# Optimization experiments

Measured on AMD Instinct MI355X. Metric: run time of the kernel, lower is better.

## Reference

```python
import jax, jax.numpy as jnp
import numpy as np

N = 10000      # num_nodes
E = 640000     # num_edges
IN = 512       # in_channels
H = 7          # GCNConv hidden/out dim (hard-coded in module)


def _glorot(key, shape):
    s = np.sqrt(6.0 / (shape[0] + shape[1])).astype(np.float32)
    return jax.random.uniform(key, shape, jnp.float32, -s, s)


def setup_inputs() -> dict:
    key = jax.random.key(0)
    k = jax.random.split(key, 6)
    x = jax.random.normal(k[0], (N, IN), jnp.float32)
    edge_index = jax.random.randint(k[1], (2, E), 0, N, dtype=jnp.int32)
    edge_attr = jax.random.uniform(k[2], (E, 1), jnp.float32)
    adj = jnp.zeros((N, N), jnp.float32)  # unused by forward, per original API
    W1 = _glorot(k[3], (IN, H))
    b1 = jnp.zeros((H,), jnp.float32)
    W2 = _glorot(k[4], (H, H))
    b2 = jnp.zeros((H,), jnp.float32)
    return {"x": x, "edge_index": edge_index, "edge_attr": edge_attr,
            "adj": adj, "W1": W1, "b1": b1, "W2": W2, "b2": b2}


def _gcn_layer(x, row, col, ew, W, b):
    n = x.shape[0]
    # add self-loops (improved=False -> loop weight 1)
    loop = jnp.arange(n, dtype=row.dtype)
    row_f = jnp.concatenate([row, loop])
    col_f = jnp.concatenate([col, loop])
    ew_f = jnp.concatenate([ew, jnp.ones((n,), x.dtype)])
    # symmetric degree normalization: deg from scatter_add on row
    deg = jax.ops.segment_sum(ew_f, row_f, num_segments=n)
    deg_inv = jnp.where(deg > 0, deg ** -0.5, 0.0).astype(x.dtype)
    norm = deg_inv[row_f] * ew_f * deg_inv[col_f]          # [E+N]
    h = x @ W                                              # [n, out]
    out = jax.ops.segment_sum(norm[:, None] * h[col_f], row_f, num_segments=n)
    return out + b


def reference(x, edge_index, edge_attr, adj, W1, b1, W2, b2):
    row, col = edge_index[0], edge_index[1]
    ew = edge_attr.reshape(-1)
    h = _gcn_layer(x, row, col, ew, W1, b1)
    h = _gcn_layer(h, row, col, ew, W2, b2)
    reg = jnp.zeros((1,), x.dtype)
    return h, reg
```

## Files before the change

kernel.cpp:

```cpp
#include <hip/hip_runtime.h>

#define NN   10000
#define NE   640000
#define IC   512
#define H    7
#define HP   8
#define NCH  256
#define CE   (NE / NCH)
#define RG   250
#define RN   40
#define CAP  3072
#define MMB  256
#define GN   32
#define NGB  ((NN + GN - 1) / GN)

__device__ __forceinline__ float wave_sum(float v) {
    #pragma unroll
    for (int off = 32; off; off >>= 1) v += __shfl_xor(v, off);
    return v;
}

__device__ __forceinline__ float group16_sum(float v) {
    #pragma unroll
    for (int off = 1; off < 16; off <<= 1) v += __shfl_xor(v, off);
    return v;
}

__global__ __launch_bounds__(1024) void k_bucket_mm1(
    const int* __restrict__ row, const int* __restrict__ col,
    const float* __restrict__ ew, const float* __restrict__ x,
    const float* __restrict__ W1, int* __restrict__ gcur,
    int2* __restrict__ gbuf, float* __restrict__ h1)
{
    __shared__ int   lhist[RG];
    __shared__ int   loffs[RG];
    __shared__ int   lbase[RG];
    __shared__ int   lcur[RG];
    __shared__ int2  st[CE];
    __shared__ float wls[IC * H];
    const int tid = threadIdx.x;

    if (blockIdx.x < NCH) {
        const int base = blockIdx.x * CE;
        if (tid < RG) lhist[tid] = 0;
        __syncthreads();
        int ex[3]; float ef[3];
        #pragma unroll
        for (int k = 0; k < 3; ++k) {
            const int i = tid + k * 1024;
            ex[k] = -1;
            if (i < CE) {
                const int e = base + i;
                const int r = row[e], c = col[e];
                const int rg = r / RN, rl = r - rg * RN;
                ex[k] = c | (rl << 14) | (rg << 20);
                ef[k] = ew[e];
                atomicAdd(&lhist[rg], 1);
            }
        }
        __syncthreads();
        if (tid < RG) lbase[tid] = tid * CAP + atomicAdd(&gcur[tid], lhist[tid]);
        if (tid < 64) {
            const int ln = tid;
            int t4[4]; int s4 = 0;
            #pragma unroll
            for (int k = 0; k < 4; ++k) {
                const int j = ln * 4 + k;
                t4[k] = (j < RG) ? lhist[j] : 0;
                s4 += t4[k];
            }
            int s = s4;
            #pragma unroll
            for (int off = 1; off < 64; off <<= 1) {
                const int t = __shfl_up(s, off);
                if (ln >= off) s += t;
            }
            int run = s - s4;
            #pragma unroll
            for (int k = 0; k < 4; ++k) {
                const int j = ln * 4 + k;
                if (j < RG) { loffs[j] = run; lcur[j] = run; }
                run += t4[k];
            }
        }
        __syncthreads();
        #pragma unroll
        for (int k = 0; k < 3; ++k) {
            if (ex[k] >= 0) {
                const int pos = atomicAdd(&lcur[ex[k] >> 20], 1);
                st[pos] = make_int2(ex[k], __float_as_int(ef[k]));
            }
        }
        __syncthreads();
        #pragma unroll
        for (int k = 0; k < 3; ++k) {
            const int i = tid + k * 1024;
            if (i < CE) {
                const int rg = st[i].x >> 20;
                gbuf[lbase[rg] + (i - loffs[rg])] = st[i];
            }
        }
    } else {
        for (int i = tid; i < IC * H; i += 1024) wls[i] = W1[i];
        __syncthreads();
        const int wv = tid >> 6, ln = tid & 63;
        const int rb = (blockIdx.x - NCH) * RN;
        for (int r0 = wv; r0 < RN; r0 += 16) {
            const int r = rb + r0;
            const float4* xr4 = (const float4*)(x + (size_t)r * IC);
            const float4 a0 = xr4[ln * 2], a1 = xr4[ln * 2 + 1];
            const float e8[8] = {a0.x, a0.y, a0.z, a0.w, a1.x, a1.y, a1.z, a1.w};
            const float* wb = &wls[ln * 8 * H];
            float acc[H] = {};
            #pragma unroll
            for (int m = 0; m < 8; ++m)
                #pragma unroll
                for (int c = 0; c < H; ++c) acc[c] += e8[m] * wb[m * H + c];
            #pragma unroll
            for (int c = 0; c < H; ++c) {
                const float v = wave_sum(acc[c]);
                if (ln == 0) h1[r * HP + c] = v;
            }
            if (ln == 0) h1[r * HP + 7] = 0.0f;
        }
    }
}

__global__ __launch_bounds__(1024) void k_sort_deg_g1(
    const int* __restrict__ gcur, int2* __restrict__ gbuf,
    const float* __restrict__ h1, float* __restrict__ dinv,
    float* __restrict__ g1, int2* __restrict__ nseg)
{
    __shared__ int   lhist[RN];
    __shared__ float ldeg[RN];
    __shared__ int   loffs[RN];
    __shared__ int   lcur[RN];
    __shared__ float ldv[RN];
    __shared__ int2  st[CAP];
    const int tid = threadIdx.x, b = blockIdx.x;
    if (tid < RN) { lhist[tid] = 0; ldeg[tid] = 0.0f; }
    __syncthreads();
    const int cnt = gcur[b];
    int2* bk = gbuf + (size_t)b * CAP;
    int2 ed[3];
    #pragma unroll
    for (int k = 0; k < 3; ++k) {
        const int i = tid + k * 1024;
        ed[k] = make_int2(-1, 0);
        if (i < cnt) {
            ed[k] = bk[i];
            const int rl = (ed[k].x >> 14) & 63;
            atomicAdd(&lhist[rl], 1);
            atomicAdd(&ldeg[rl], __int_as_float(ed[k].y));
        }
    }
    __syncthreads();
    if (tid < 64) {
        int v = (tid < RN) ? lhist[tid] : 0;
        int s = v;
        #pragma unroll
        for (int off = 1; off < 64; off <<= 1) {
            const int t = __shfl_up(s, off);
            if (tid >= off) s += t;
        }
        if (tid < RN) { loffs[tid] = s - v; lcur[tid] = s - v; }
    } else if (tid >= 64 && tid < 64 + RN) {
        ldv[tid - 64] = rsqrtf(1.0f + ldeg[tid - 64]);
    }
    __syncthreads();
    #pragma unroll
    for (int k = 0; k < 3; ++k) {
        if (ed[k].x >= 0) {
            const int rl = (ed[k].x >> 14) & 63;
            const int pos = atomicAdd(&lcur[rl], 1);
            st[pos] = ed[k];
        }
    }
    __syncthreads();
    #pragma unroll
    for (int k = 0; k < 3; ++k) {
        const int i = tid + k * 1024;
        if (i < cnt) bk[i] = st[i];
    }
    if (tid < RN) {
        dinv[b * RN + tid] = ldv[tid];
        nseg[b * RN + tid] = make_int2(loffs[tid], lhist[tid]);
    }
    if (tid < RN * HP) {
        const int n = tid >> 3;
        g1[(size_t)(b * RN) * HP + tid] = ldv[n] * h1[(size_t)(b * RN) * HP + tid];
    }
}

template <bool FUSE_MM2>
__global__ __launch_bounds__(512) void k_gather(
    const int* __restrict__ gcur_unused, const int2* __restrict__ gbuf,
    const int2* __restrict__ nseg, const float* __restrict__ dinv,
    const float* __restrict__ g, const float* __restrict__ bias,
    const float* __restrict__ W2, float* __restrict__ out)
{
    __shared__ float asum[GN][HP];
    __shared__ float vals[GN][HP];
    __shared__ float ldv[GN];
    __shared__ float w2[H * H];
    __shared__ float bb[H];
    const int tid = threadIdx.x, b = blockIdx.x;
    const int gid = tid >> 4, q = tid & 15;
    const int gn = b * GN + gid;
    if (!FUSE_MM2 && b == 0 && tid == 511) out[(size_t)NN * H] = 0.0f;
    if (tid < GN && b * GN + tid < NN) ldv[tid] = dinv[b * GN + tid];
    if (FUSE_MM2 && tid >= 64 && tid < 64 + H * H) w2[tid - 64] = W2[tid - 64];
    if (tid >= 128 && tid < 128 + H) bb[tid - 128] = bias[tid - 128];
    __syncthreads();
    if (gn < NN) {
        const int2 seg = nseg[gn];
        const int2* bk = gbuf + (size_t)(gn / RN) * CAP;
        const int kend = seg.x + seg.y;
        float acc[H] = {};
        for (int k = seg.x + q; k < kend; k += 32) {
            const int k2i = k + 16;
            const int2 e0 = bk[k];
            const int2 e1 = bk[k2i < kend ? k2i : k];
            const float w0 = __int_as_float(e0.y);
            const float w1 = (k2i < kend) ? __int_as_float(e1.y) : 0.0f;
            const float4* p0 = (const float4*)(g + (size_t)(e0.x & 16383) * HP);
            const float4* p1 = (const float4*)(g + (size_t)(e1.x & 16383) * HP);
            const float4 lo0 = p0[0], hi0 = p0[1];
            const float4 lo1 = p1[0], hi1 = p1[1];
            acc[0] += w0 * lo0.x + w1 * lo1.x;
            acc[1] += w0 * lo0.y + w1 * lo1.y;
            acc[2] += w0 * lo0.z + w1 * lo1.z;
            acc[3] += w0 * lo0.w + w1 * lo1.w;
            acc[4] += w0 * hi0.x + w1 * hi1.x;
            acc[5] += w0 * hi0.y + w1 * hi1.y;
            acc[6] += w0 * hi0.z + w1 * hi1.z;
        }
        #pragma unroll
        for (int j = 0; j < H; ++j) {
            const float s = group16_sum(acc[j]);
            if (q == 0) asum[gid][j] = s;
        }
    }
    __syncthreads();
    if (tid < GN * H) {
        const int n = tid / H, k = tid - n * H;
        const int node = b * GN + n;
        if (node < NN)
            vals[n][k] = ldv[n] * (asum[n][k] + g[(size_t)node * HP + k]) + bb[k];
    }
    __syncthreads();
    if (tid < GN * H) {
        const int n = tid / H, k = tid - n * H;
        const int node = b * GN + n;
        if (node < NN) {
            if (FUSE_MM2) {
                float o = 0.0f;
                #pragma unroll
                for (int j = 0; j < H; ++j) o += vals[n][j] * w2[j * H + k];
                out[(size_t)node * HP + k] = ldv[n] * o;
            } else {
                out[(size_t)node * H + k] = vals[n][k];
            }
        }
    }
    if (FUSE_MM2 && tid >= 256 && tid < 256 + GN) {
        const int node = b * GN + (tid - 256);
        if (node < NN) out[(size_t)node * HP + 7] = 0.0f;
    }
}

extern "C" void kernel_launch(void* const* d_in, const int* in_sizes, int n_in,
                              void* d_out, int out_size, void* d_ws, size_t ws_size,
                              hipStream_t stream) {
    const float* x  = (const float*)d_in[0];
    const int*   ei = (const int*)d_in[1];
    const float* ea = (const float*)d_in[2];
    const float* W1 = (const float*)d_in[4];
    const float* b1 = (const float*)d_in[5];
    const float* W2 = (const float*)d_in[6];
    const float* b2 = (const float*)d_in[7];
    float* out = (float*)d_out;

    char* p = (char*)d_ws;
    int* gcur = (int*)p;          p += 1024;
    int2* gbuf = (int2*)p;        p += sizeof(int2) * RG * CAP;
    int2* nseg = (int2*)p;        p += sizeof(int2) * NN;
    float* h1 = (float*)p;        p += sizeof(float) * NN * HP;
    float* g1 = (float*)p;        p += sizeof(float) * NN * HP;
    float* g2 = (float*)p;        p += sizeof(float) * NN * HP;
    float* dinv = (float*)p;      p += sizeof(float) * NN;

    const int* row = ei;
    const int* col = ei + NE;

    hipMemsetAsync(gcur, 0, RG * sizeof(int), stream);
    k_bucket_mm1<<<NCH + MMB, 1024, 0, stream>>>(row, col, ea, x, W1, gcur, gbuf, h1);
    k_sort_deg_g1<<<RG, 1024, 0, stream>>>(gcur, gbuf, h1, dinv, g1, nseg);
    k_gather<true><<<NGB, 512, 0, stream>>>(gcur, gbuf, nseg, dinv, g1, b1, W2, g2);
    k_gather<false><<<NGB, 512, 0, stream>>>(gcur, gbuf, nseg, dinv, g2, b2, nullptr, out);
}
```

Before: 54.97 us.

## Replace global atomic bucket append with per-chunk histograms and pull-side staging

The first kernel no longer does global atomicAdd on per-bucket cursors and scattered writes. Each chunk now writes its locally sorted edges contiguously, plus a per-chunk histogram and offset table. The second kernel gathers its bucket's slices from all 256 chunks into shared memory, using a prefix sum over the chunk counts, before the existing local sort. This removes the memset launch and the global atomics, but adds an extra NE-sized buffer, a strided histogram read, and short, uncoalesced per-chunk copies (four threads per chunk) in the sort kernel.

```diff
diff --git a/kernel.cpp b/kernel.cpp
--- a/kernel.cpp
+++ b/kernel.cpp
@@ -29,12 +29,12 @@
 __global__ __launch_bounds__(1024) void k_bucket_mm1(
     const int* __restrict__ row, const int* __restrict__ col,
     const float* __restrict__ ew, const float* __restrict__ x,
-    const float* __restrict__ W1, int* __restrict__ gcur,
-    int2* __restrict__ gbuf, float* __restrict__ h1)
+    const float* __restrict__ W1, int* __restrict__ ghist,
+    int* __restrict__ goffs, int2* __restrict__ gbuf2,
+    float* __restrict__ h1)
 {
     __shared__ int   lhist[RG];
     __shared__ int   loffs[RG];
-    __shared__ int   lbase[RG];
     __shared__ int   lcur[RG];
     __shared__ int2  st[CE];
     __shared__ float wls[IC * H];
@@ -59,7 +59,6 @@
             }
         }
         __syncthreads();
-        if (tid < RG) lbase[tid] = tid * CAP + atomicAdd(&gcur[tid], lhist[tid]);
         if (tid < 64) {
             const int ln = tid;
             int t4[4]; int s4 = 0;
@@ -95,10 +94,11 @@
         #pragma unroll
         for (int k = 0; k < 3; ++k) {
             const int i = tid + k * 1024;
-            if (i < CE) {
-                const int rg = st[i].x >> 20;
-                gbuf[lbase[rg] + (i - loffs[rg])] = st[i];
-            }
+            if (i < CE) gbuf2[base + i] = st[i];
+        }
+        if (tid < RG) {
+            ghist[blockIdx.x * RG + tid] = lhist[tid];
+            goffs[blockIdx.x * RG + tid] = loffs[tid];
         }
     } else {
         for (int i = tid; i < IC * H; i += 1024) wls[i] = W1[i];
@@ -107,6 +107,7 @@
         const int rb = (blockIdx.x - NCH) * RN;
         for (int r0 = wv; r0 < RN; r0 += 16) {
             const int r = rb + r0;
+            if (r >= NN) break;
             const float4* xr4 = (const float4*)(x + (size_t)r * IC);
             const float4 a0 = xr4[ln * 2], a1 = xr4[ln * 2 + 1];
             const float e8[8] = {a0.x, a0.y, a0.z, a0.w, a1.x, a1.y, a1.z, a1.w};
@@ -127,28 +128,58 @@
 }
 
 __global__ __launch_bounds__(1024) void k_sort_deg_g1(
-    const int* __restrict__ gcur, int2* __restrict__ gbuf,
-    const float* __restrict__ h1, float* __restrict__ dinv,
-    float* __restrict__ g1, int2* __restrict__ nseg)
+    const int* __restrict__ ghist, const int* __restrict__ goffs,
+    const int2* __restrict__ gbuf2, const float* __restrict__ h1,
+    float* __restrict__ dinv, float* __restrict__ g1,
+    int2* __restrict__ nseg, int2* __restrict__ gbuf)
 {
+    __shared__ int2  staged[CAP];
+    __shared__ int2  st2[CAP];
+    __shared__ int   ccnt[NCH];
+    __shared__ int   coff[NCH];
+    __shared__ int   total_s;
     __shared__ int   lhist[RN];
     __shared__ float ldeg[RN];
     __shared__ int   loffs[RN];
     __shared__ int   lcur[RN];
     __shared__ float ldv[RN];
-    __shared__ int2  st[CAP];
     const int tid = threadIdx.x, b = blockIdx.x;
-    if (tid < RN) { lhist[tid] = 0; ldeg[tid] = 0.0f; }
-    __syncthreads();
-    const int cnt = gcur[b];
-    int2* bk = gbuf + (size_t)b * CAP;
+
+    if (tid < NCH) ccnt[tid] = ghist[tid * RG + b];
+    if (tid >= 256 && tid < 256 + RN) { lhist[tid - 256] = 0; ldeg[tid - 256] = 0.0f; }
+    __syncthreads();
+    if (tid < 64) {
+        const int ln = tid;
+        int t4[4]; int s4 = 0;
+        #pragma unroll
+        for (int k = 0; k < 4; ++k) { t4[k] = ccnt[ln * 4 + k]; s4 += t4[k]; }
+        int s = s4;
+        #pragma unroll
+        for (int off = 1; off < 64; off <<= 1) {
+            const int t = __shfl_up(s, off);
+            if (ln >= off) s += t;
+        }
+        int run = s - s4;
+        #pragma unroll
+        for (int k = 0; k < 4; ++k) { coff[ln * 4 + k] = run; run += t4[k]; }
+        if (ln == 63) total_s = run;
+    }
+    __syncthreads();
+    {
+        const int c = tid >> 2;
+        const int cn = ccnt[c], co = coff[c];
+        const int src = c * CE + goffs[c * RG + b];
+        for (int i = tid & 3; i < cn; i += 4) staged[co + i] = gbuf2[src + i];
+    }
+    __syncthreads();
+    const int cnt = total_s;
     int2 ed[3];
     #pragma unroll
     for (int k = 0; k < 3; ++k) {
         const int i = tid + k * 1024;
         ed[k] = make_int2(-1, 0);
         if (i < cnt) {
-            ed[k] = bk[i];
+            ed[k] = staged[i];
             const int rl = (ed[k].x >> 14) & 63;
             atomicAdd(&lhist[rl], 1);
             atomicAdd(&ldeg[rl], __int_as_float(ed[k].y));
@@ -173,14 +204,14 @@
         if (ed[k].x >= 0) {
             const int rl = (ed[k].x >> 14) & 63;
             const int pos = atomicAdd(&lcur[rl], 1);
-            st[pos] = ed[k];
+            st2[pos] = ed[k];
         }
     }
     __syncthreads();
     #pragma unroll
     for (int k = 0; k < 3; ++k) {
         const int i = tid + k * 1024;
-        if (i < cnt) bk[i] = st[i];
+        if (i < cnt) gbuf[(size_t)b * CAP + i] = st2[i];
     }
     if (tid < RN) {
         dinv[b * RN + tid] = ldv[tid];
@@ -194,10 +225,10 @@
 
 template <bool FUSE_MM2>
 __global__ __launch_bounds__(512) void k_gather(
-    const int* __restrict__ gcur_unused, const int2* __restrict__ gbuf,
-    const int2* __restrict__ nseg, const float* __restrict__ dinv,
-    const float* __restrict__ g, const float* __restrict__ bias,
-    const float* __restrict__ W2, float* __restrict__ out)
+    const int2* __restrict__ gbuf, const int2* __restrict__ nseg,
+    const float* __restrict__ dinv, const float* __restrict__ g,
+    const float* __restrict__ bias, const float* __restrict__ W2,
+    float* __restrict__ out)
 {
     __shared__ float asum[GN][HP];
     __shared__ float vals[GN][HP];
@@ -282,7 +313,9 @@
     float* out = (float*)d_out;
 
     char* p = (char*)d_ws;
-    int* gcur = (int*)p;          p += 1024;
+    int* ghist = (int*)p;         p += sizeof(int) * NCH * RG;
+    int* goffs = (int*)p;         p += sizeof(int) * NCH * RG;
+    int2* gbuf2 = (int2*)p;       p += sizeof(int2) * NE;
     int2* gbuf = (int2*)p;        p += sizeof(int2) * RG * CAP;
     int2* nseg = (int2*)p;        p += sizeof(int2) * NN;
     float* h1 = (float*)p;        p += sizeof(float) * NN * HP;
@@ -293,9 +326,10 @@
     const int* row = ei;
     const int* col = ei + NE;
 
-    hipMemsetAsync(gcur, 0, RG * sizeof(int), stream);
-    k_bucket_mm1<<<NCH + MMB, 1024, 0, stream>>>(row, col, ea, x, W1, gcur, gbuf, h1);
-    k_sort_deg_g1<<<RG, 1024, 0, stream>>>(gcur, gbuf, h1, dinv, g1, nseg);
-    k_gather<true><<<NGB, 512, 0, stream>>>(gcur, gbuf, nseg, dinv, g1, b1, W2, g2);
-    k_gather<false><<<NGB, 512, 0, stream>>>(gcur, gbuf, nseg, dinv, g2, b2, nullptr, out);
-}
+    k_bucket_mm1<<<NCH + MMB, 1024, 0, stream>>>(row, col, ea, x, W1,
+                                                 ghist, goffs, gbuf2, h1);
+    k_sort_deg_g1<<<RG, 1024, 0, stream>>>(ghist, goffs, gbuf2, h1,
+                                           dinv, g1, nseg, gbuf);
+    k_gather<true><<<NGB, 512, 0, stream>>>(gbuf, nseg, dinv, g1, b1, W2, g2);
+    k_gather<false><<<NGB, 512, 0, stream>>>(gbuf, nseg, dinv, g2, b2, nullptr, out);
+}
```

Result: faster. 47.84 us (-13.0%).
